# Optimization experiments

Hardware: AMD Instinct MI355X
Metric: run time of the kernel (lower is better)

Reference implementation:

```python
import jax, jax.numpy as jnp
import numpy as np

B, S, D = 2, 512, 2048          # batch, seq, hidden
H, Dh = 16, 128                 # heads, head_dim
E, K, G, TG = 8, 2, 2, 1        # experts, top_k, n_group, topk_group
I, IS = 1024, 1024              # routed / shared expert intermediate
ROUTED_SCALE = 2.5
EPS = 1e-6
ROPE_THETA = 10000.0


def setup_inputs() -> dict:
    key = jax.random.key(0)
    ks = jax.random.split(key, 13)
    p = lambda k, shape, s=0.02: jax.random.normal(k, shape, jnp.float32) * s
    return {
        "hidden_states": jax.random.normal(ks[0], (B, S, D), jnp.float32),
        "ln1_w": jnp.ones((D,), jnp.float32),
        "ln2_w": jnp.ones((D,), jnp.float32),
        "wq": p(ks[1], (D, H * Dh)),
        "wk": p(ks[2], (D, H * Dh)),
        "wv": p(ks[3], (D, H * Dh)),
        "wo": p(ks[4], (H * Dh, D)),
        "gate_w": p(ks[5], (E, D)),
        "gate_bias": p(ks[6], (E,), 0.1),
        "w_gate": p(ks[7], (E, D, I)),
        "w_up": p(ks[8], (E, D, I)),
        "w_down": p(ks[9], (E, I, D)),
        "sw_gate": p(ks[10], (D, IS)),
        "sw_up": p(ks[11], (D, IS)),
        "sw_down": p(ks[12], (IS, D)),
    }


def _rmsnorm(x, w):
    var = jnp.mean(x * x, axis=-1, keepdims=True)
    return x * jax.lax.rsqrt(var + EPS) * w


def _rope_cos_sin(seq_len):
    inv_freq = 1.0 / (ROPE_THETA ** (jnp.arange(0, Dh, 2, dtype=jnp.float32) / Dh))
    ang = jnp.arange(seq_len, dtype=jnp.float32)[:, None] * inv_freq  # [S, Dh/2]
    return jnp.cos(ang)[None, :, None, :], jnp.sin(ang)[None, :, None, :]


def _apply_rope(x, cos, sin):
    x1, x2 = jnp.split(x, 2, axis=-1)
    return jnp.concatenate([x1 * cos - x2 * sin, x2 * cos + x1 * sin], axis=-1)


def _attention(x, wq, wk, wv, wo):
    q = (x @ wq).reshape(B, S, H, Dh)
    k = (x @ wk).reshape(B, S, H, Dh)
    v = (x @ wv).reshape(B, S, H, Dh)
    cos, sin = _rope_cos_sin(S)
    q = _apply_rope(q, cos, sin)
    k = _apply_rope(k, cos, sin)
    scores = jnp.einsum('bqhd,bkhd->bhqk', q, k) * (1.0 / np.sqrt(Dh).astype(np.float32))
    causal = jnp.tril(jnp.ones((S, S), bool))
    scores = jnp.where(causal, scores, jnp.finfo(scores.dtype).min)
    attn = jax.nn.softmax(scores, axis=-1)
    out = jnp.einsum('bhqk,bkhd->bqhd', attn, v).reshape(B, S, H * Dh)
    return out @ wo


def _moe(x, gate_w, gate_bias, w_gate, w_up, w_down, sw_gate, sw_up, sw_down):
    # x: [T, D]. noaux_tc grouped top-k routing (DeepSeek-V3 style).
    T = x.shape[0]
    logits = x @ gate_w.T                      # [T, E]
    scores = jax.nn.sigmoid(logits)
    sc = scores + gate_bias                    # selection scores with correction bias
    grp = sc.reshape(T, G, E // G)
    group_scores = jnp.sum(jax.lax.top_k(grp, 2)[0], axis=-1)  # top-2 sum per group [T,G]
    _, gidx = jax.lax.top_k(group_scores, TG)
    gmask = jnp.zeros((T, G), bool).at[jnp.arange(T)[:, None], gidx].set(True)
    emask = jnp.broadcast_to(gmask[:, :, None], (T, G, E // G)).reshape(T, E)
    masked = jnp.where(emask, sc, -jnp.inf)
    _, idx = jax.lax.top_k(masked, K)          # [T, K] expert ids
    w = jnp.take_along_axis(scores, idx, axis=-1)
    w = w / jnp.sum(w, axis=-1, keepdims=True)  # norm_topk_prob=True
    # dense combine weights [T, E] (zero except K entries per token)
    cw = jnp.zeros((T, E), x.dtype).at[jnp.arange(T)[:, None], idx].add(w)

    def body(acc, xs):
        wg, wu, wd, cwe = xs
        y = (jax.nn.silu(x @ wg) * (x @ wu)) @ wd  # SiluAndMul gated MLP
        return acc + cwe[:, None] * y, None

    routed, _ = jax.lax.scan(body, jnp.zeros_like(x), (w_gate, w_up, w_down, cw.T))
    shared = (jax.nn.silu(x @ sw_gate) * (x @ sw_up)) @ sw_down
    return routed * ROUTED_SCALE + shared


def reference(hidden_states, ln1_w, ln2_w, wq, wk, wv, wo, gate_w, gate_bias,
              w_gate, w_up, w_down, sw_gate, sw_up, sw_down):
    h = hidden_states
    h = h + _attention(_rmsnorm(h, ln1_w), wq, wk, wv, wo)
    x = _rmsnorm(h, ln2_w).reshape(B * S, D)
    moe_out = _moe(x, gate_w, gate_bias, w_gate, w_up, w_down,
                   sw_gate, sw_up, sw_down).reshape(B, S, D)
    return h + moe_out
```

## Files before the change

### kernel.cpp

```cpp
#include <hip/hip_runtime.h>

typedef __bf16 bf16x4 __attribute__((ext_vector_type(4)));
typedef __bf16 bf16x8 __attribute__((ext_vector_type(8)));
typedef float  f32x4  __attribute__((ext_vector_type(4)));

#define THREADS 256
constexpr int BK = 32, BKP = 40;

constexpr size_t MB = 1024*1024;
constexpr size_t oH2    = 0;
constexpr size_t oXB2   = 8*MB;
constexpr size_t oRT    = 12*MB;
constexpr size_t oWQKVT = 16*MB;
constexpr size_t oWQKVL = 40*MB;
constexpr size_t oWOT   = 64*MB;
constexpr size_t oWOL   = 72*MB;
constexpr size_t oXN1   = 80*MB;
constexpr size_t oXN1L  = 84*MB;
constexpr size_t oQKV   = 88*MB;
constexpr size_t oSCF   = 112*MB;
constexpr size_t oQKS   = 144*MB;
constexpr size_t oQKSL  = 152*MB;
constexpr size_t oVT    = 16*MB;
constexpr size_t oVTL   = 20*MB;
constexpr size_t oATT   = 24*MB;
constexpr size_t oPB    = 40*MB;
constexpr size_t oPBL2  = 88*MB;
constexpr size_t oWGUT  = 16*MB;
constexpr size_t oWDT   = 80*MB;
constexpr size_t oSGUT  = 112*MB;
constexpr size_t oSDT   = 120*MB;
constexpr size_t oGU    = 124*MB;
constexpr size_t oHB    = 140*MB;
constexpr size_t oY     = 144*MB;
constexpr size_t oSGU   = 16*MB;
constexpr size_t oSHB   = 24*MB;
constexpr size_t oSDB   = 26*MB;
constexpr size_t oEIDX = oRT;
constexpr size_t oEW   = oRT + 8192;
constexpr size_t oSLOT = oRT + 16384;
constexpr size_t oLIST = oRT + 24576;
constexpr size_t oCNT  = oRT + 32768;
constexpr size_t oOFF  = oRT + 33024;
constexpr size_t oCUR  = oRT + 33280;

__device__ __forceinline__ bf16x8 bzero8() {
  bf16x8 z;
#pragma unroll
  for (int j = 0; j < 8; ++j) z[j] = (__bf16)0.f;
  return z;
}

template<int OM>
__global__ void transpose_kernel(const float* __restrict__ in, __bf16* __restrict__ out,
                                 int ldin, int ldout, int zlo,
                                 long inBH, long inBL, long outB, long plane) {
  __shared__ float tile[64][65];
  int z = blockIdx.z;
  const float* inp = in + (long)(z / zlo) * inBH + (long)(z % zlo) * inBL;
  __bf16* outp = out + (long)z * outB;
  int r0 = blockIdx.y * 64, c0 = blockIdx.x * 64;
  int tid = threadIdx.x;
#pragma unroll
  for (int i = 0; i < 4; ++i) {
    int lin = tid + i * 256;
    int r = lin >> 4, c4 = (lin & 15) << 2;
    f32x4 v = *(const f32x4*)(inp + (long)(r0 + r) * ldin + c0 + c4);
    tile[r][c4] = v[0]; tile[r][c4+1] = v[1]; tile[r][c4+2] = v[2]; tile[r][c4+3] = v[3];
  }
  __syncthreads();
#pragma unroll
  for (int i = 0; i < 4; ++i) {
    int lin = tid + i * 256;
    int oR = lin >> 4, oC4 = (lin & 15) << 2;
    bf16x4 hi, lo;
#pragma unroll
    for (int j = 0; j < 4; ++j) {
      float v = tile[oC4 + j][oR];
      hi[j] = (__bf16)v;
      if constexpr (OM == 2) lo[j] = (__bf16)(v - (float)hi[j]);
    }
    __bf16* dst = outp + (long)(c0 + oR) * ldout + r0 + oC4;
    *(bf16x4*)dst = hi;
    if constexpr (OM == 2) *(bf16x4*)(dst + plane) = lo;
  }
}

template<int MODE, int SP, bool RESID, bool CAUSAL, bool KTRI, int TBM = 128, int TBN = 128>
__global__ __launch_bounds__(256, 2)
void gemm_kernel(const void* __restrict__ Av, const void* __restrict__ Bv, float* __restrict__ C,
                 const float* __restrict__ Rres,
                 int M, int N, int K, int lda, int ldb, int ldc,
                 int zlo, long aHi, long aLo, long bHi, long bLo, long cHi, long cLo,
                 long aPlane, long bPlane,
                 const int* __restrict__ counts, const int* __restrict__ offsets,
                 const int* __restrict__ gather) {
  const int n0 = blockIdx.x * TBN;
  const int m0 = blockIdx.y * TBM;
  const int z  = blockIdx.z;
  if (CAUSAL && n0 > m0) return;

  const float*  Af = (const float*)Av;
  const __bf16* Ah = (const __bf16*)Av;
  const __bf16* Bh = (const __bf16*)Bv;

  int mcount; int rowbase = 0;
  long aoff = 0, boff = 0, coff = 0;
  if constexpr (MODE == 0) {
    mcount = M;
    int zh = z / zlo, zl = z % zlo;
    aoff = (long)zh*aHi + (long)zl*aLo;
    boff = (long)zh*bHi + (long)zl*bLo;
    coff = (long)zh*cHi + (long)zl*cLo;
  } else {
    mcount = counts[z];
    rowbase = offsets[z];
    if (m0 >= mcount) return;
    boff = (long)z*bHi;
  }

  constexpr bool TRI = (SP != 0);
  constexpr int ABUF = TBM*BKP;
  constexpr int BBUF = TBN*BKP;
  constexpr int WTM = TBM/2, WTN = TBN/2;
  constexpr int MI = WTM/16, MJ = WTN/16;
  __shared__ __align__(16) __bf16 As[(TRI?2:1)*ABUF];
  __shared__ __align__(16) __bf16 Bs[(TRI?2:1)*BBUF];

  const int tid = threadIdx.x;
  const int lane = tid & 63, wave = tid >> 6;
  const int wm = wave >> 1, wn = wave & 1;
  const int lq = lane >> 4, lr = lane & 15;

  int kend = K;
  if (KTRI) { int ke = m0 + TBM; kend = ke < K ? ke : K; }

  f32x4 acc[MI][MJ] = {};

  constexpr int NAF = (SP==1) ? TBM/32 : 1;
  constexpr int NAH = (SP!=1) ? TBM/64 : 1;
  constexpr int NB  = TBN/64;
  f32x4  arf[NAF];
  bf16x8 arh[NAH], arl[NAH];
  bf16x8 brh[NB],  brl[NB];

  auto loadAB = [&](int kk) {
    if constexpr (SP == 1) {
#pragma unroll
      for (int it = 0; it < NAF; ++it) {
        int lin = tid + it*THREADS;
        int row = lin >> 3, c4 = (lin & 7) << 2;
        int gr = m0 + row;
        f32x4 zv; zv[0]=0.f; zv[1]=0.f; zv[2]=0.f; zv[3]=0.f;
        arf[it] = (gr < mcount) ? *(const f32x4*)(Af + aoff + (long)gr*lda + kk + c4) : zv;
      }
    } else {
#pragma unroll
      for (int it = 0; it < NAH; ++it) {
        int lin = tid + it*THREADS;
        int row = lin >> 2, c8 = (lin & 3) << 3;
        int gr = m0 + row;
        arh[it] = bzero8();
        if constexpr (SP == 2) arl[it] = bzero8();
        if (gr < mcount) {
          long arow;
          if constexpr (MODE == 1) arow = gather[rowbase + gr];
          else if constexpr (MODE == 2) arow = rowbase + gr;
          else arow = gr;
          const __bf16* p = Ah + aoff + arow*(long)lda + kk + c8;
          arh[it] = *(const bf16x8*)p;
          if constexpr (SP == 2) arl[it] = *(const bf16x8*)(p + aPlane);
        }
      }
    }
#pragma unroll
    for (int it = 0; it < NB; ++it) {
      int lin = tid + it*THREADS;
      int row = lin >> 2, c8 = (lin & 3) << 3;
      const __bf16* p = Bh + boff + (long)(n0+row)*ldb + kk + c8;
      brh[it] = *(const bf16x8*)p;
      if constexpr (TRI) brl[it] = *(const bf16x8*)(p + bPlane);
    }
  };

  auto writeAB = [&]() {
    if constexpr (SP == 1) {
#pragma unroll
      for (int it = 0; it < NAF; ++it) {
        int lin = tid + it*THREADS;
        int row = lin >> 3, c4 = (lin & 7) << 2;
        bf16x4 hi, lo;
#pragma unroll
        for (int j = 0; j < 4; ++j) {
          hi[j] = (__bf16)arf[it][j];
          lo[j] = (__bf16)(arf[it][j] - (float)hi[j]);
        }
        *(bf16x4*)(As + row*BKP + c4) = hi;
        *(bf16x4*)(As + ABUF + row*BKP + c4) = lo;
      }
    } else {
#pragma unroll
      for (int it = 0; it < NAH; ++it) {
        int lin = tid + it*THREADS;
        int row = lin >> 2, c8 = (lin & 3) << 3;
        *(bf16x8*)(As + row*BKP + c8) = arh[it];
        if constexpr (SP == 2) *(bf16x8*)(As + ABUF + row*BKP + c8) = arl[it];
      }
    }
#pragma unroll
    for (int it = 0; it < NB; ++it) {
      int lin = tid + it*THREADS;
      int row = lin >> 2, c8 = (lin & 3) << 3;
      *(bf16x8*)(Bs + row*BKP + c8) = brh[it];
      if constexpr (TRI) *(bf16x8*)(Bs + BBUF + row*BKP + c8) = brl[it];
    }
  };

  loadAB(0);
  writeAB();
  __syncthreads();

  for (int k0 = 0; k0 < kend; k0 += BK) {
    const bool hn = (k0 + BK < kend);
    if (hn) loadAB(k0 + BK);

    bf16x8 fa[MI], fal[MI];
    const __bf16* ap = As + (wm*WTM + lr)*BKP + lq*8;
    const __bf16* bp = Bs + (wn*WTN + lr)*BKP + lq*8;
#pragma unroll
    for (int i = 0; i < MI; ++i) {
      fa[i] = *(const bf16x8*)(ap + i*16*BKP);
      if constexpr (TRI) fal[i] = *(const bf16x8*)(ap + ABUF + i*16*BKP);
    }
#pragma unroll
    for (int j = 0; j < MJ; ++j) {
      bf16x8 fb = *(const bf16x8*)(bp + j*16*BKP);
      if constexpr (TRI) {
        bf16x8 fbl = *(const bf16x8*)(bp + BBUF + j*16*BKP);
#pragma unroll
        for (int i = 0; i < MI; ++i) {
          acc[i][j] = __builtin_amdgcn_mfma_f32_16x16x32_bf16(fa[i],  fbl, acc[i][j], 0, 0, 0);
          acc[i][j] = __builtin_amdgcn_mfma_f32_16x16x32_bf16(fal[i], fb,  acc[i][j], 0, 0, 0);
          acc[i][j] = __builtin_amdgcn_mfma_f32_16x16x32_bf16(fa[i],  fb,  acc[i][j], 0, 0, 0);
        }
      } else {
#pragma unroll
        for (int i = 0; i < MI; ++i)
          acc[i][j] = __builtin_amdgcn_mfma_f32_16x16x32_bf16(fa[i], fb, acc[i][j], 0, 0, 0);
      }
    }

    if (hn) {
      __syncthreads();
      writeAB();
      __syncthreads();
    }
  }

#pragma unroll
  for (int i = 0; i < MI; ++i) {
#pragma unroll
    for (int rg = 0; rg < 4; ++rg) {
      int lrow = wm*WTM + i*16 + lq*4 + rg;
      int gr = m0 + lrow;
      if (gr < mcount) {
        long crow = coff + (long)(rowbase + gr)*ldc;
#pragma unroll
        for (int j = 0; j < MJ; ++j) {
          int col = n0 + wn*WTN + j*16 + lr;
          float val = acc[i][j][rg];
          if constexpr (RESID) val += Rres[(long)gr*ldc + col];
          C[crow + col] = val;
        }
      }
    }
  }
}

template<int OM>
__global__ void rmsnorm_kernel(const float* __restrict__ x, const float* __restrict__ w,
                               __bf16* __restrict__ out, long plane) {
  const int row = blockIdx.x;
  const float* xr = x + (long)row * 2048;
  float ss = 0.f;
  for (int d = threadIdx.x; d < 2048; d += 256) { float v = xr[d]; ss += v*v; }
  __shared__ float red[4];
  int lane = threadIdx.x & 63, wave = threadIdx.x >> 6;
#pragma unroll
  for (int off = 32; off; off >>= 1) ss += __shfl_down(ss, off, 64);
  if (lane == 0) red[wave] = ss;
  __syncthreads();
  float tot = red[0] + red[1] + red[2] + red[3];
  float rs = rsqrtf(tot * (1.f/2048.f) + 1e-6f);
  __bf16* orow = out + (long)row * 2048;
  for (int d = threadIdx.x; d < 2048; d += 256) {
    float v = xr[d]*rs*w[d];
    __bf16 h = (__bf16)v;
    orow[d] = h;
    if constexpr (OM == 2) orow[d + plane] = (__bf16)(v - (float)h);
  }
}

__global__ void rope_split_kernel(const float* __restrict__ qkv, __bf16* __restrict__ o, long plane) {
  int tid = blockIdx.x*256 + threadIdx.x;
  int i = tid & 63;
  int th = tid >> 6;
  int h = th & 15;
  int t = th >> 4;
  int s = t & 511;
  long ib = (long)t*6144 + h*128;
  long ob = (long)t*4096 + h*128;
  float inv = 1.f / powf(10000.f, (float)i * (1.f/64.f));
  float ang = (float)s * inv;
  float c = cosf(ang), sn = sinf(ang);
  float q1 = qkv[ib+i], q2 = qkv[ib+64+i];
  float r1 = q1*c - q2*sn, r2 = q2*c + q1*sn;
  __bf16 h1 = (__bf16)r1, h2v = (__bf16)r2;
  o[ob+i] = h1;            o[ob+i+plane] = (__bf16)(r1 - (float)h1);
  o[ob+64+i] = h2v;        o[ob+64+i+plane] = (__bf16)(r2 - (float)h2v);
  float k1 = qkv[ib+2048+i], k2 = qkv[ib+2048+64+i];
  float s1 = k1*c - k2*sn, s2 = k2*c + k1*sn;
  __bf16 g1 = (__bf16)s1, g2 = (__bf16)s2;
  o[ob+2048+i] = g1;       o[ob+2048+i+plane] = (__bf16)(s1 - (float)g1);
  o[ob+2048+64+i] = g2;    o[ob+2048+64+i+plane] = (__bf16)(s2 - (float)g2);
}

__global__ void softmax_kernel(const float* __restrict__ sc, __bf16* __restrict__ p, long plane) {
  int r = blockIdx.x & 511;
  long bh = blockIdx.x >> 9;
  const float scale = 0.08838834764831845f;
  long base = (bh*512 + r)*512;
  int c0 = threadIdx.x, c1 = threadIdx.x + 256;
  float v0 = (c0 <= r) ? sc[base+c0]*scale : -3.0e38f;
  float v1 = (c1 <= r) ? sc[base+c1]*scale : -3.0e38f;
  float m = fmaxf(v0, v1);
  __shared__ float red[4];
  int lane = threadIdx.x & 63, wave = threadIdx.x >> 6;
#pragma unroll
  for (int off = 32; off; off >>= 1) m = fmaxf(m, __shfl_xor(m, off, 64));
  if (lane == 0) red[wave] = m;
  __syncthreads();
  m = fmaxf(fmaxf(red[0], red[1]), fmaxf(red[2], red[3]));
  __syncthreads();
  float e0 = (c0 <= r) ? expf(v0 - m) : 0.f;
  float e1 = (c1 <= r) ? expf(v1 - m) : 0.f;
  float s = e0 + e1;
#pragma unroll
  for (int off = 32; off; off >>= 1) s += __shfl_xor(s, off, 64);
  if (lane == 0) red[wave] = s;
  __syncthreads();
  s = red[0] + red[1] + red[2] + red[3];
  float inv = 1.f / s;
  float p0 = e0*inv, p1 = e1*inv;
  __bf16 h0 = (__bf16)p0, h1 = (__bf16)p1;
  p[base+c0] = h0; p[base+c0+plane] = (__bf16)(p0 - (float)h0);
  p[base+c1] = h1; p[base+c1+plane] = (__bf16)(p1 - (float)h1);
}

__global__ void zero8_kernel(int* c) { if (threadIdx.x < 8) c[threadIdx.x] = 0; }

__global__ void routing_kernel(const float* __restrict__ h2, const float* __restrict__ ln2w,
                               const float* __restrict__ gw, const float* __restrict__ gb,
                               int* __restrict__ eidx, float* __restrict__ ew,
                               int* __restrict__ counts) {
  int t = blockIdx.x;
  const float* xr = h2 + (long)t*2048;
  int lane = threadIdx.x & 63, wave = threadIdx.x >> 6;
  float ss = 0.f;
  for (int d = threadIdx.x; d < 2048; d += 256) { float v = xr[d]; ss += v*v; }
  __shared__ float red[4];
#pragma unroll
  for (int off = 32; off; off >>= 1) ss += __shfl_down(ss, off, 64);
  if (lane == 0) red[wave] = ss;
  __syncthreads();
  float rs = rsqrtf((red[0]+red[1]+red[2]+red[3]) * (1.f/2048.f) + 1e-6f);
  __shared__ float lg[8];
  for (int e = wave; e < 8; e += 4) {
    const float* wr = gw + (long)e*2048;
    float acc = 0.f;
    for (int d = lane; d < 2048; d += 64) acc += (xr[d]*rs*ln2w[d]) * wr[d];
#pragma unroll
    for (int off = 32; off; off >>= 1) acc += __shfl_down(acc, off, 64);
    if (lane == 0) lg[e] = acc;
  }
  __syncthreads();
  if (threadIdx.x == 0) {
    float sg[8], sc[8];
#pragma unroll
    for (int e = 0; e < 8; ++e) { sg[e] = 1.f/(1.f+expf(-lg[e])); sc[e] = sg[e] + gb[e]; }
    float gs[2];
#pragma unroll
    for (int g = 0; g < 2; ++g) {
      float m1 = -3e38f, m2 = -3e38f;
#pragma unroll
      for (int j = 0; j < 4; ++j) {
        float v = sc[4*g+j];
        if (v > m1) { m2 = m1; m1 = v; } else if (v > m2) m2 = v;
      }
      gs[g] = m1 + m2;
    }
    int b4 = (gs[1] > gs[0]) ? 4 : 0;
    int i1 = 0; float v1 = -3e38f;
#pragma unroll
    for (int j = 0; j < 4; ++j) if (sc[b4+j] > v1) { v1 = sc[b4+j]; i1 = j; }
    int i2 = -1; float v2 = -3e38f;
#pragma unroll
    for (int j = 0; j < 4; ++j) if (j != i1 && sc[b4+j] > v2) { v2 = sc[b4+j]; i2 = j; }
    float w1 = sg[b4+i1], w2 = sg[b4+i2], s = w1 + w2;
    eidx[t*2] = b4+i1; eidx[t*2+1] = b4+i2;
    ew[t*2] = w1/s;    ew[t*2+1] = w2/s;
    atomicAdd(&counts[b4+i1], 1); atomicAdd(&counts[b4+i2], 1);
  }
}

__global__ void scan_kernel(const int* __restrict__ counts, int* __restrict__ offsets,
                            int* __restrict__ cursors) {
  if (threadIdx.x == 0 && blockIdx.x == 0) {
    int s = 0;
    for (int e = 0; e < 8; ++e) { offsets[e] = s; s += counts[e]; cursors[e] = 0; }
    offsets[8] = s;
  }
}

__global__ void scatter_kernel(const int* __restrict__ eidx, const int* __restrict__ offsets,
                               int* __restrict__ cursors, int* __restrict__ list,
                               int* __restrict__ slot) {
  int t = blockIdx.x*256 + threadIdx.x;
  if (t < 1024) {
#pragma unroll
    for (int kk = 0; kk < 2; ++kk) {
      int e = eidx[t*2+kk];
      int pos = atomicAdd(&cursors[e], 1);
      int g = offsets[e] + pos;
      list[g] = t;
      slot[t*2+kk] = g;
    }
  }
}

__global__ void silumul_kernel(const float* __restrict__ gu, __bf16* __restrict__ o, int n) {
  int i = blockIdx.x*256 + threadIdx.x;
  if (i < n) {
    int s = i >> 10, j = i & 1023;
    float gv = gu[(long)s*2048 + j];
    float uv = gu[(long)s*2048 + 1024 + j];
    float sg = gv / (1.f + expf(-gv));
    o[i] = (__bf16)(sg * uv);
  }
}

__global__ void combine_kernel(const float* __restrict__ h2, const float* __restrict__ y,
                               const float* __restrict__ sdown, const int* __restrict__ slot,
                               const float* __restrict__ ew, float* __restrict__ out) {
  int i = blockIdx.x*256 + threadIdx.x;
  int t = i >> 11;
  int d = i & 2047;
  float rv = ew[t*2]   * y[(long)slot[t*2]  *2048 + d]
           + ew[t*2+1] * y[(long)slot[t*2+1]*2048 + d];
  out[i] = h2[i] + sdown[i] + 2.5f * rv;
}

extern "C" void kernel_launch(void* const* d_in, const int* in_sizes, int n_in,
                              void* d_out, int out_size, void* d_ws, size_t ws_size,
                              hipStream_t stream) {
  const float* hid  = (const float*)d_in[0];
  const float* ln1  = (const float*)d_in[1];
  const float* ln2  = (const float*)d_in[2];
  const float* wq   = (const float*)d_in[3];
  const float* wk   = (const float*)d_in[4];
  const float* wv   = (const float*)d_in[5];
  const float* wo   = (const float*)d_in[6];
  const float* gw   = (const float*)d_in[7];
  const float* gb   = (const float*)d_in[8];
  const float* wgat = (const float*)d_in[9];
  const float* wup  = (const float*)d_in[10];
  const float* wdn  = (const float*)d_in[11];
  const float* swg  = (const float*)d_in[12];
  const float* swu  = (const float*)d_in[13];
  const float* swd  = (const float*)d_in[14];
  float* out = (float*)d_out;
  char* ws = (char*)d_ws;

  float*  h2    = (float*)(ws + oH2);
  __bf16* xb2   = (__bf16*)(ws + oXB2);
  __bf16* wqkvT = (__bf16*)(ws + oWQKVT);
  __bf16* woT   = (__bf16*)(ws + oWOT);
  __bf16* xn1   = (__bf16*)(ws + oXN1);
  float*  qkv   = (float*)(ws + oQKV);
  float*  scf   = (float*)(ws + oSCF);
  __bf16* qks   = (__bf16*)(ws + oQKS);
  __bf16* vtb   = (__bf16*)(ws + oVT);
  float*  att   = (float*)(ws + oATT);
  __bf16* pb    = (__bf16*)(ws + oPB);
  __bf16* wgut  = (__bf16*)(ws + oWGUT);
  __bf16* wdt   = (__bf16*)(ws + oWDT);
  __bf16* sgut  = (__bf16*)(ws + oSGUT);
  __bf16* sdt   = (__bf16*)(ws + oSDT);
  float*  gu    = (float*)(ws + oGU);
  __bf16* hb    = (__bf16*)(ws + oHB);
  float*  ybuf  = (float*)(ws + oY);
  float*  sgu   = (float*)(ws + oSGU);
  __bf16* shb   = (__bf16*)(ws + oSHB);
  float*  sdb   = (float*)(ws + oSDB);
  int*   eidx = (int*)(ws + oEIDX);
  float* ew   = (float*)(ws + oEW);
  int*   slot = (int*)(ws + oSLOT);
  int*   list = (int*)(ws + oLIST);
  int*   cnt  = (int*)(ws + oCNT);
  int*   offs = (int*)(ws + oOFF);
  int*   curs = (int*)(ws + oCUR);

  const long S22 = (long)2048*2048, S21 = (long)2048*1024;
  const long pWQKV = (oWQKVL - oWQKVT) / 2;
  const long pWO   = (oWOL - oWOT) / 2;
  const long pXN1  = 2*MB;
  const long pQKS  = (oQKSL - oQKS) / 2;
  const long pVT   = 2*MB;
  const long pPB   = (oPBL2 - oPB) / 2;

  transpose_kernel<2><<<dim3(32,32,1), 256, 0, stream>>>(wq, wqkvT,          2048, 2048, 1, 0, 0, 0, pWQKV);
  transpose_kernel<2><<<dim3(32,32,1), 256, 0, stream>>>(wk, wqkvT + S22,    2048, 2048, 1, 0, 0, 0, pWQKV);
  transpose_kernel<2><<<dim3(32,32,1), 256, 0, stream>>>(wv, wqkvT + 2*S22,  2048, 2048, 1, 0, 0, 0, pWQKV);
  transpose_kernel<2><<<dim3(32,32,1), 256, 0, stream>>>(wo, woT,            2048, 2048, 1, 0, 0, 0, pWO);

  rmsnorm_kernel<2><<<1024, 256, 0, stream>>>(hid, ln1, xn1, pXN1);

  gemm_kernel<0, 2, false, false, false, 64, 128><<<dim3(48,16,1), 256, 0, stream>>>(
      xn1, wqkvT, qkv, nullptr, 1024, 6144, 2048, 2048, 2048, 6144,
      1, 0, 0, 0, 0, 0, 0, pXN1, pWQKV, nullptr, nullptr, nullptr);

  rope_split_kernel<<<4096, 256, 0, stream>>>(qkv, qks, pQKS);

  transpose_kernel<2><<<dim3(2,8,32), 256, 0, stream>>>(
      qkv + 4096, vtb, 6144, 512, 16, (long)512*6144, 128, (long)128*512, pVT);

  gemm_kernel<0, 2, false, true, false, 64, 64><<<dim3(8,8,32), 256, 0, stream>>>(
      qks, qks + 2048, scf, nullptr, 512, 512, 128, 4096, 4096, 512,
      16, (long)512*4096, 128, (long)512*4096, 128, (long)16*512*512, (long)512*512,
      pQKS, pQKS, nullptr, nullptr, nullptr);

  softmax_kernel<<<16384, 256, 0, stream>>>(scf, pb, pPB);

  gemm_kernel<0, 2, false, false, true, 64, 64><<<dim3(2,8,32), 256, 0, stream>>>(
      pb, vtb, att, nullptr, 512, 128, 512, 512, 512, 2048,
      16, (long)16*512*512, (long)512*512, (long)16*128*512, (long)128*512,
      (long)512*2048, 128, pPB, pVT, nullptr, nullptr, nullptr);

  gemm_kernel<0, 1, true, false, false, 64, 64><<<dim3(32,16,1), 256, 0, stream>>>(
      att, woT, h2, hid, 1024, 2048, 2048, 2048, 2048, 2048,
      1, 0, 0, 0, 0, 0, 0, 0, pWO, nullptr, nullptr, nullptr);

  rmsnorm_kernel<1><<<1024, 256, 0, stream>>>(h2, ln2, xb2, 0);
  zero8_kernel<<<1, 64, 0, stream>>>(cnt);
  routing_kernel<<<1024, 256, 0, stream>>>(h2, ln2, gw, gb, eidx, ew, cnt);
  scan_kernel<<<1, 64, 0, stream>>>(cnt, offs, curs);
  scatter_kernel<<<4, 256, 0, stream>>>(eidx, offs, curs, list, slot);

  transpose_kernel<1><<<dim3(16,32,8), 256, 0, stream>>>(wgat, wgut,        1024, 2048, 1, S21, 0, S22, 0);
  transpose_kernel<1><<<dim3(16,32,8), 256, 0, stream>>>(wup,  wgut + S21,  1024, 2048, 1, S21, 0, S22, 0);
  transpose_kernel<1><<<dim3(32,16,8), 256, 0, stream>>>(wdn,  wdt,         2048, 1024, 1, S21, 0, S21, 0);
  transpose_kernel<1><<<dim3(16,32,1), 256, 0, stream>>>(swg,  sgut,        1024, 2048, 1, 0, 0, 0, 0);
  transpose_kernel<1><<<dim3(16,32,1), 256, 0, stream>>>(swu,  sgut + S21,  1024, 2048, 1, 0, 0, 0, 0);
  transpose_kernel<1><<<dim3(32,16,1), 256, 0, stream>>>(swd,  sdt,         2048, 1024, 1, 0, 0, 0, 0);

  gemm_kernel<1, 0, false, false, false, 64, 64><<<dim3(32,16,8), 256, 0, stream>>>(
      xb2, wgut, gu, nullptr, 1024, 2048, 2048, 2048, 2048, 2048,
      1, 0, 0, S22, 0, 0, 0, 0, 0, cnt, offs, list);
  silumul_kernel<<<8192, 256, 0, stream>>>(gu, hb, 2048*1024);
  gemm_kernel<2, 0, false, false, false, 64, 64><<<dim3(32,16,8), 256, 0, stream>>>(
      hb, wdt, ybuf, nullptr, 1024, 2048, 1024, 1024, 1024, 2048,
      1, 0, 0, S21, 0, 0, 0, 0, 0, cnt, offs, nullptr);

  gemm_kernel<0, 0, false, false, false, 64, 64><<<dim3(32,16,1), 256, 0, stream>>>(
      xb2, sgut, sgu, nullptr, 1024, 2048, 2048, 2048, 2048, 2048,
      1, 0, 0, 0, 0, 0, 0, 0, 0, nullptr, nullptr, nullptr);
  silumul_kernel<<<4096, 256, 0, stream>>>(sgu, shb, 1024*1024);
  gemm_kernel<0, 0, false, false, false, 64, 64><<<dim3(32,16,1), 256, 0, stream>>>(
      shb, sdt, sdb, nullptr, 1024, 2048, 1024, 1024, 1024, 2048,
      1, 0, 0, 0, 0, 0, 0, 0, 0, nullptr, nullptr, nullptr);

  combine_kernel<<<8192, 256, 0, stream>>>(h2, ybuf, sdb, slot, ew, out);
}
```

Baseline: 760.1 us.

## Use fp16 single-pass GEMMs for QKV/O, fuse SiLU-mul into gate/up GEMM

The QKV and output projections switch from a three-pass split-bf16 scheme (hi/lo planes, 3 MFMAs per step) to a single fp16 MFMA pass with fp16 weights and activations. This removes the lo planes and two thirds of the MFMA work, at some cost in accuracy. The gate/up projections for the routed and shared experts move into a new kernel that computes both accumulators and writes SiLU(g)*u as bf16. That drops the fp32 intermediate buffer and the separate silumul kernels. The second RMSNorm is also folded into the routing kernel, which now writes the normalized bf16 activations itself.

```diff
diff --git a/kernel.cpp b/kernel.cpp
--- a/kernel.cpp
+++ b/kernel.cpp
@@ -2,6 +2,8 @@
 
 typedef __bf16 bf16x4 __attribute__((ext_vector_type(4)));
 typedef __bf16 bf16x8 __attribute__((ext_vector_type(8)));
+typedef _Float16 f16x4 __attribute__((ext_vector_type(4)));
+typedef _Float16 f16x8 __attribute__((ext_vector_type(8)));
 typedef float  f32x4  __attribute__((ext_vector_type(4)));
 
 #define THREADS 256
@@ -12,11 +14,8 @@
 constexpr size_t oXB2   = 8*MB;
 constexpr size_t oRT    = 12*MB;
 constexpr size_t oWQKVT = 16*MB;
-constexpr size_t oWQKVL = 40*MB;
 constexpr size_t oWOT   = 64*MB;
-constexpr size_t oWOL   = 72*MB;
 constexpr size_t oXN1   = 80*MB;
-constexpr size_t oXN1L  = 84*MB;
 constexpr size_t oQKV   = 88*MB;
 constexpr size_t oSCF   = 112*MB;
 constexpr size_t oQKS   = 144*MB;
@@ -30,10 +29,8 @@
 constexpr size_t oWDT   = 80*MB;
 constexpr size_t oSGUT  = 112*MB;
 constexpr size_t oSDT   = 120*MB;
-constexpr size_t oGU    = 124*MB;
 constexpr size_t oHB    = 140*MB;
 constexpr size_t oY     = 144*MB;
-constexpr size_t oSGU   = 16*MB;
 constexpr size_t oSHB   = 24*MB;
 constexpr size_t oSDB   = 26*MB;
 constexpr size_t oEIDX = oRT;
@@ -73,16 +70,23 @@
   for (int i = 0; i < 4; ++i) {
     int lin = tid + i * 256;
     int oR = lin >> 4, oC4 = (lin & 15) << 2;
-    bf16x4 hi, lo;
-#pragma unroll
-    for (int j = 0; j < 4; ++j) {
-      float v = tile[oC4 + j][oR];
-      hi[j] = (__bf16)v;
-      if constexpr (OM == 2) lo[j] = (__bf16)(v - (float)hi[j]);
-    }
     __bf16* dst = outp + (long)(c0 + oR) * ldout + r0 + oC4;
-    *(bf16x4*)dst = hi;
-    if constexpr (OM == 2) *(bf16x4*)(dst + plane) = lo;
+    if constexpr (OM == 3) {
+      f16x4 hv;
+#pragma unroll
+      for (int j = 0; j < 4; ++j) hv[j] = (_Float16)tile[oC4 + j][oR];
+      *reinterpret_cast<f16x4*>(dst) = hv;
+    } else {
+      bf16x4 hi, lo;
+#pragma unroll
+      for (int j = 0; j < 4; ++j) {
+        float v = tile[oC4 + j][oR];
+        hi[j] = (__bf16)v;
+        if constexpr (OM == 2) lo[j] = (__bf16)(v - (float)hi[j]);
+      }
+      *(bf16x4*)dst = hi;
+      if constexpr (OM == 2) *(bf16x4*)(dst + plane) = lo;
+    }
   }
 }
 
@@ -119,7 +123,9 @@
     boff = (long)z*bHi;
   }
 
-  constexpr bool TRI = (SP != 0);
+  constexpr bool TRI  = (SP == 1 || SP == 2);
+  constexpr bool F16  = (SP == 3 || SP == 4);
+  constexpr bool AFLY = (SP == 1 || SP == 4);
   constexpr int ABUF = TBM*BKP;
   constexpr int BBUF = TBN*BKP;
   constexpr int WTM = TBM/2, WTN = TBN/2;
@@ -137,15 +143,15 @@
 
   f32x4 acc[MI][MJ] = {};
 
-  constexpr int NAF = (SP==1) ? TBM/32 : 1;
-  constexpr int NAH = (SP!=1) ? TBM/64 : 1;
+  constexpr int NAF = AFLY ? TBM/32 : 1;
+  constexpr int NAH = (!AFLY) ? TBM/64 : 1;
   constexpr int NB  = TBN/64;
   f32x4  arf[NAF];
   bf16x8 arh[NAH], arl[NAH];
   bf16x8 brh[NB],  brl[NB];
 
   auto loadAB = [&](int kk) {
-    if constexpr (SP == 1) {
+    if constexpr (AFLY) {
 #pragma unroll
       for (int it = 0; it < NAF; ++it) {
         int lin = tid + it*THREADS;
@@ -184,19 +190,26 @@
   };
 
   auto writeAB = [&]() {
-    if constexpr (SP == 1) {
+    if constexpr (AFLY) {
 #pragma unroll
       for (int it = 0; it < NAF; ++it) {
         int lin = tid + it*THREADS;
         int row = lin >> 3, c4 = (lin & 7) << 2;
-        bf16x4 hi, lo;
-#pragma unroll
-        for (int j = 0; j < 4; ++j) {
-          hi[j] = (__bf16)arf[it][j];
-          lo[j] = (__bf16)(arf[it][j] - (float)hi[j]);
+        if constexpr (SP == 4) {
+          f16x4 hv;
+#pragma unroll
+          for (int j = 0; j < 4; ++j) hv[j] = (_Float16)arf[it][j];
+          *reinterpret_cast<f16x4*>(As + row*BKP + c4) = hv;
+        } else {
+          bf16x4 hi, lo;
+#pragma unroll
+          for (int j = 0; j < 4; ++j) {
+            hi[j] = (__bf16)arf[it][j];
+            lo[j] = (__bf16)(arf[it][j] - (float)hi[j]);
+          }
+          *(bf16x4*)(As + row*BKP + c4) = hi;
+          *(bf16x4*)(As + ABUF + row*BKP + c4) = lo;
         }
-        *(bf16x4*)(As + row*BKP + c4) = hi;
-        *(bf16x4*)(As + ABUF + row*BKP + c4) = lo;
       }
     } else {
 #pragma unroll
@@ -224,29 +237,43 @@
     const bool hn = (k0 + BK < kend);
     if (hn) loadAB(k0 + BK);
 
-    bf16x8 fa[MI], fal[MI];
     const __bf16* ap = As + (wm*WTM + lr)*BKP + lq*8;
     const __bf16* bp = Bs + (wn*WTN + lr)*BKP + lq*8;
-#pragma unroll
-    for (int i = 0; i < MI; ++i) {
-      fa[i] = *(const bf16x8*)(ap + i*16*BKP);
-      if constexpr (TRI) fal[i] = *(const bf16x8*)(ap + ABUF + i*16*BKP);
-    }
-#pragma unroll
-    for (int j = 0; j < MJ; ++j) {
-      bf16x8 fb = *(const bf16x8*)(bp + j*16*BKP);
-      if constexpr (TRI) {
-        bf16x8 fbl = *(const bf16x8*)(bp + BBUF + j*16*BKP);
-#pragma unroll
-        for (int i = 0; i < MI; ++i) {
-          acc[i][j] = __builtin_amdgcn_mfma_f32_16x16x32_bf16(fa[i],  fbl, acc[i][j], 0, 0, 0);
-          acc[i][j] = __builtin_amdgcn_mfma_f32_16x16x32_bf16(fal[i], fb,  acc[i][j], 0, 0, 0);
-          acc[i][j] = __builtin_amdgcn_mfma_f32_16x16x32_bf16(fa[i],  fb,  acc[i][j], 0, 0, 0);
+    if constexpr (F16) {
+      f16x8 fa[MI];
+#pragma unroll
+      for (int i = 0; i < MI; ++i)
+        fa[i] = *reinterpret_cast<const f16x8*>(ap + i*16*BKP);
+#pragma unroll
+      for (int j = 0; j < MJ; ++j) {
+        f16x8 fb = *reinterpret_cast<const f16x8*>(bp + j*16*BKP);
+#pragma unroll
+        for (int i = 0; i < MI; ++i)
+          acc[i][j] = __builtin_amdgcn_mfma_f32_16x16x32_f16(fa[i], fb, acc[i][j], 0, 0, 0);
+      }
+    } else {
+      bf16x8 fa[MI], fal[MI];
+#pragma unroll
+      for (int i = 0; i < MI; ++i) {
+        fa[i] = *(const bf16x8*)(ap + i*16*BKP);
+        if constexpr (TRI) fal[i] = *(const bf16x8*)(ap + ABUF + i*16*BKP);
+      }
+#pragma unroll
+      for (int j = 0; j < MJ; ++j) {
+        bf16x8 fb = *(const bf16x8*)(bp + j*16*BKP);
+        if constexpr (TRI) {
+          bf16x8 fbl = *(const bf16x8*)(bp + BBUF + j*16*BKP);
+#pragma unroll
+          for (int i = 0; i < MI; ++i) {
+            acc[i][j] = __builtin_amdgcn_mfma_f32_16x16x32_bf16(fa[i],  fbl, acc[i][j], 0, 0, 0);
+            acc[i][j] = __builtin_amdgcn_mfma_f32_16x16x32_bf16(fal[i], fb,  acc[i][j], 0, 0, 0);
+            acc[i][j] = __builtin_amdgcn_mfma_f32_16x16x32_bf16(fa[i],  fb,  acc[i][j], 0, 0, 0);
+          }
+        } else {
+#pragma unroll
+          for (int i = 0; i < MI; ++i)
+            acc[i][j] = __builtin_amdgcn_mfma_f32_16x16x32_bf16(fa[i], fb, acc[i][j], 0, 0, 0);
         }
-      } else {
-#pragma unroll
-        for (int i = 0; i < MI; ++i)
-          acc[i][j] = __builtin_amdgcn_mfma_f32_16x16x32_bf16(fa[i], fb, acc[i][j], 0, 0, 0);
       }
     }
 
@@ -271,6 +298,117 @@
           float val = acc[i][j][rg];
           if constexpr (RESID) val += Rres[(long)gr*ldc + col];
           C[crow + col] = val;
+        }
+      }
+    }
+  }
+}
+
+template<int MODE>
+__global__ __launch_bounds__(256, 2)
+void gugemm_kernel(const __bf16* __restrict__ A, const __bf16* __restrict__ B,
+                   __bf16* __restrict__ O, int M, int K, int lda, int ldb, long bHi,
+                   const int* __restrict__ counts, const int* __restrict__ offsets,
+                   const int* __restrict__ gather) {
+  const int n0 = blockIdx.x * 64;
+  const int m0 = blockIdx.y * 64;
+  const int z  = blockIdx.z;
+
+  int mcount; int rowbase = 0; long boff = 0;
+  if constexpr (MODE == 1) {
+    mcount = counts[z];
+    rowbase = offsets[z];
+    if (m0 >= mcount) return;
+    boff = (long)z*bHi;
+  } else {
+    mcount = M;
+  }
+
+  constexpr int TBUF = 64*BKP;
+  __shared__ __align__(16) __bf16 As[TBUF];
+  __shared__ __align__(16) __bf16 Bg[TBUF];
+  __shared__ __align__(16) __bf16 Bu[TBUF];
+
+  const int tid = threadIdx.x;
+  const int lane = tid & 63, wave = tid >> 6;
+  const int wm = wave >> 1, wn = wave & 1;
+  const int lq = lane >> 4, lr = lane & 15;
+
+  f32x4 accG[2][2] = {}, accU[2][2] = {};
+
+  bf16x8 ar, bg, bu;
+  const int srow = tid >> 2, sc8 = (tid & 3) << 3;
+  long aBase; bool aOK;
+  {
+    int gr = m0 + srow;
+    aOK = gr < mcount;
+    long arow = 0;
+    if (aOK) {
+      if constexpr (MODE == 1) arow = gather[rowbase + gr];
+      else arow = gr;
+    }
+    aBase = arow*(long)lda;
+  }
+  const long gBase = boff + (long)(n0 + srow)*ldb;
+  const long uBase = boff + (long)(1024 + n0 + srow)*ldb;
+
+  auto loadAB = [&](int kk) {
+    ar = aOK ? *(const bf16x8*)(A + aBase + kk + sc8) : bzero8();
+    bg = *(const bf16x8*)(B + gBase + kk + sc8);
+    bu = *(const bf16x8*)(B + uBase + kk + sc8);
+  };
+  auto writeAB = [&]() {
+    *(bf16x8*)(As + srow*BKP + sc8) = ar;
+    *(bf16x8*)(Bg + srow*BKP + sc8) = bg;
+    *(bf16x8*)(Bu + srow*BKP + sc8) = bu;
+  };
+
+  loadAB(0);
+  writeAB();
+  __syncthreads();
+
+  for (int k0 = 0; k0 < K; k0 += BK) {
+    const bool hn = (k0 + BK < K);
+    if (hn) loadAB(k0 + BK);
+
+    const __bf16* ap  = As + (wm*32 + lr)*BKP + lq*8;
+    const __bf16* bgp = Bg + (wn*32 + lr)*BKP + lq*8;
+    const __bf16* bup = Bu + (wn*32 + lr)*BKP + lq*8;
+    bf16x8 fa[2];
+    fa[0] = *(const bf16x8*)(ap);
+    fa[1] = *(const bf16x8*)(ap + 16*BKP);
+#pragma unroll
+    for (int j = 0; j < 2; ++j) {
+      bf16x8 fg = *(const bf16x8*)(bgp + j*16*BKP);
+      bf16x8 fu = *(const bf16x8*)(bup + j*16*BKP);
+#pragma unroll
+      for (int i = 0; i < 2; ++i) {
+        accG[i][j] = __builtin_amdgcn_mfma_f32_16x16x32_bf16(fa[i], fg, accG[i][j], 0, 0, 0);
+        accU[i][j] = __builtin_amdgcn_mfma_f32_16x16x32_bf16(fa[i], fu, accU[i][j], 0, 0, 0);
+      }
+    }
+
+    if (hn) {
+      __syncthreads();
+      writeAB();
+      __syncthreads();
+    }
+  }
+
+#pragma unroll
+  for (int i = 0; i < 2; ++i) {
+#pragma unroll
+    for (int rg = 0; rg < 4; ++rg) {
+      int lrow = wm*32 + i*16 + lq*4 + rg;
+      int gr = m0 + lrow;
+      if (gr < mcount) {
+        long orow = (long)(rowbase + gr)*1024;
+#pragma unroll
+        for (int j = 0; j < 2; ++j) {
+          int col = n0 + wn*32 + j*16 + lr;
+          float g = accG[i][j][rg], u = accU[i][j][rg];
+          float val = (g / (1.f + expf(-g))) * u;
+          O[orow + col] = (__bf16)val;
         }
       }
     }
@@ -295,9 +433,13 @@
   __bf16* orow = out + (long)row * 2048;
   for (int d = threadIdx.x; d < 2048; d += 256) {
     float v = xr[d]*rs*w[d];
-    __bf16 h = (__bf16)v;
-    orow[d] = h;
-    if constexpr (OM == 2) orow[d + plane] = (__bf16)(v - (float)h);
+    if constexpr (OM == 3) {
+      ((_Float16*)orow)[d] = (_Float16)v;
+    } else {
+      __bf16 h = (__bf16)v;
+      orow[d] = h;
+      if constexpr (OM == 2) orow[d + plane] = (__bf16)(v - (float)h);
+    }
   }
 }
 
@@ -361,6 +503,7 @@
 
 __global__ void routing_kernel(const float* __restrict__ h2, const float* __restrict__ ln2w,
                                const float* __restrict__ gw, const float* __restrict__ gb,
+                               __bf16* __restrict__ xb2,
                                int* __restrict__ eidx, float* __restrict__ ew,
                                int* __restrict__ counts) {
   int t = blockIdx.x;
@@ -374,6 +517,8 @@
   if (lane == 0) red[wave] = ss;
   __syncthreads();
   float rs = rsqrtf((red[0]+red[1]+red[2]+red[3]) * (1.f/2048.f) + 1e-6f);
+  __bf16* xrow = xb2 + (long)t*2048;
+  for (int d = threadIdx.x; d < 2048; d += 256) xrow[d] = (__bf16)(xr[d]*rs*ln2w[d]);
   __shared__ float lg[8];
   for (int e = wave; e < 8; e += 4) {
     const float* wr = gw + (long)e*2048;
@@ -435,17 +580,6 @@
       list[g] = t;
       slot[t*2+kk] = g;
     }
-  }
-}
-
-__global__ void silumul_kernel(const float* __restrict__ gu, __bf16* __restrict__ o, int n) {
-  int i = blockIdx.x*256 + threadIdx.x;
-  if (i < n) {
-    int s = i >> 10, j = i & 1023;
-    float gv = gu[(long)s*2048 + j];
-    float uv = gu[(long)s*2048 + 1024 + j];
-    float sg = gv / (1.f + expf(-gv));
-    o[i] = (__bf16)(sg * uv);
   }
 }
 
@@ -496,10 +630,8 @@
   __bf16* wdt   = (__bf16*)(ws + oWDT);
   __bf16* sgut  = (__bf16*)(ws + oSGUT);
   __bf16* sdt   = (__bf16*)(ws + oSDT);
-  float*  gu    = (float*)(ws + oGU);
   __bf16* hb    = (__bf16*)(ws + oHB);
   float*  ybuf  = (float*)(ws + oY);
-  float*  sgu   = (float*)(ws + oSGU);
   __bf16* shb   = (__bf16*)(ws + oSHB);
   float*  sdb   = (float*)(ws + oSDB);
   int*   eidx = (int*)(ws + oEIDX);
@@ -511,23 +643,20 @@
   int*   curs = (int*)(ws + oCUR);
 
   const long S22 = (long)2048*2048, S21 = (long)2048*1024;
-  const long pWQKV = (oWQKVL - oWQKVT) / 2;
-  const long pWO   = (oWOL - oWOT) / 2;
-  const long pXN1  = 2*MB;
   const long pQKS  = (oQKSL - oQKS) / 2;
   const long pVT   = 2*MB;
   const long pPB   = (oPBL2 - oPB) / 2;
 
-  transpose_kernel<2><<<dim3(32,32,1), 256, 0, stream>>>(wq, wqkvT,          2048, 2048, 1, 0, 0, 0, pWQKV);
-  transpose_kernel<2><<<dim3(32,32,1), 256, 0, stream>>>(wk, wqkvT + S22,    2048, 2048, 1, 0, 0, 0, pWQKV);
-  transpose_kernel<2><<<dim3(32,32,1), 256, 0, stream>>>(wv, wqkvT + 2*S22,  2048, 2048, 1, 0, 0, 0, pWQKV);
-  transpose_kernel<2><<<dim3(32,32,1), 256, 0, stream>>>(wo, woT,            2048, 2048, 1, 0, 0, 0, pWO);
-
-  rmsnorm_kernel<2><<<1024, 256, 0, stream>>>(hid, ln1, xn1, pXN1);
-
-  gemm_kernel<0, 2, false, false, false, 64, 128><<<dim3(48,16,1), 256, 0, stream>>>(
+  transpose_kernel<3><<<dim3(32,32,1), 256, 0, stream>>>(wq, wqkvT,          2048, 2048, 1, 0, 0, 0, 0);
+  transpose_kernel<3><<<dim3(32,32,1), 256, 0, stream>>>(wk, wqkvT + S22,    2048, 2048, 1, 0, 0, 0, 0);
+  transpose_kernel<3><<<dim3(32,32,1), 256, 0, stream>>>(wv, wqkvT + 2*S22,  2048, 2048, 1, 0, 0, 0, 0);
+  transpose_kernel<3><<<dim3(32,32,1), 256, 0, stream>>>(wo, woT,            2048, 2048, 1, 0, 0, 0, 0);
+
+  rmsnorm_kernel<3><<<1024, 256, 0, stream>>>(hid, ln1, xn1, 0);
+
+  gemm_kernel<0, 3, false, false, false, 64, 128><<<dim3(48,16,1), 256, 0, stream>>>(
       xn1, wqkvT, qkv, nullptr, 1024, 6144, 2048, 2048, 2048, 6144,
-      1, 0, 0, 0, 0, 0, 0, pXN1, pWQKV, nullptr, nullptr, nullptr);
+      1, 0, 0, 0, 0, 0, 0, 0, 0, nullptr, nullptr, nullptr);
 
   rope_split_kernel<<<4096, 256, 0, stream>>>(qkv, qks, pQKS);
 
@@ -546,13 +675,12 @@
       16, (long)16*512*512, (long)512*512, (long)16*128*512, (long)128*512,
       (long)512*2048, 128, pPB, pVT, nullptr, nullptr, nullptr);
 
-  gemm_kernel<0, 1, true, false, false, 64, 64><<<dim3(32,16,1), 256, 0, stream>>>(
+  gemm_kernel<0, 4, true, false, false, 64, 64><<<dim3(32,16,1), 256, 0, stream>>>(
       att, woT, h2, hid, 1024, 2048, 2048, 2048, 2048, 2048,
-      1, 0, 0, 0, 0, 0, 0, 0, pWO, nullptr, nullptr, nullptr);
-
-  rmsnorm_kernel<1><<<1024, 256, 0, stream>>>(h2, ln2, xb2, 0);
+      1, 0, 0, 0, 0, 0, 0, 0, 0, nullptr, nullptr, nullptr);
+
   zero8_kernel<<<1, 64, 0, stream>>>(cnt);
-  routing_kernel<<<1024, 256, 0, stream>>>(h2, ln2, gw, gb, eidx, ew, cnt);
+  routing_kernel<<<1024, 256, 0, stream>>>(h2, ln2, gw, gb, xb2, eidx, ew, cnt);
   scan_kernel<<<1, 64, 0, stream>>>(cnt, offs, curs);
   scatter_kernel<<<4, 256, 0, stream>>>(eidx, offs, curs, list, slot);
 
@@ -563,18 +691,14 @@
   transpose_kernel<1><<<dim3(16,32,1), 256, 0, stream>>>(swu,  sgut + S21,  1024, 2048, 1, 0, 0, 0, 0);
   transpose_kernel<1><<<dim3(32,16,1), 256, 0, stream>>>(swd,  sdt,         2048, 1024, 1, 0, 0, 0, 0);
 
-  gemm_kernel<1, 0, false, false, false, 64, 64><<<dim3(32,16,8), 256, 0, stream>>>(
-      xb2, wgut, gu, nullptr, 1024, 2048, 2048, 2048, 2048, 2048,
-      1, 0, 0, S22, 0, 0, 0, 0, 0, cnt, offs, list);
-  silumul_kernel<<<8192, 256, 0, stream>>>(gu, hb, 2048*1024);
+  gugemm_kernel<1><<<dim3(16,16,8), 256, 0, stream>>>(
+      xb2, wgut, hb, 1024, 2048, 2048, 2048, S22, cnt, offs, list);
   gemm_kernel<2, 0, false, false, false, 64, 64><<<dim3(32,16,8), 256, 0, stream>>>(
       hb, wdt, ybuf, nullptr, 1024, 2048, 1024, 1024, 1024, 2048,
       1, 0, 0, S21, 0, 0, 0, 0, 0, cnt, offs, nullptr);
 
-  gemm_kernel<0, 0, false, false, false, 64, 64><<<dim3(32,16,1), 256, 0, stream>>>(
-      xb2, sgut, sgu, nullptr, 1024, 2048, 2048, 2048, 2048, 2048,
-      1, 0, 0, 0, 0, 0, 0, 0, 0, nullptr, nullptr, nullptr);
-  silumul_kernel<<<4096, 256, 0, stream>>>(sgu, shb, 1024*1024);
+  gugemm_kernel<0><<<dim3(16,16,1), 256, 0, stream>>>(
+      xb2, sgut, shb, 1024, 2048, 2048, 2048, 0, nullptr, nullptr, nullptr);
   gemm_kernel<0, 0, false, false, false, 64, 64><<<dim3(32,16,1), 256, 0, stream>>>(
       shb, sdt, sdb, nullptr, 1024, 2048, 1024, 1024, 1024, 2048,
       1, 0, 0, 0, 0, 0, 0, 0, 0, nullptr, nullptr, nullptr);
```

Measured after the change: 706.1 us. 7.1% less time.
